# Kernel optimization log

Measured on AMD Instinct MI355X. Metric: run time of the kernel, lower is better.

The kernel has to match this reference:

```python
import jax, jax.numpy as jnp
import numpy as np

GROUPS = 32
EPS = 1e-5


def setup_inputs() -> dict:
    key = jax.random.key(0)
    ks = jax.random.split(key, 8)
    B, C, H, W = 4, 512, 64, 64
    s = 1.0 / np.sqrt(C)  # conv1x1 fan-in init scale
    return {
        "x": jax.random.normal(ks[0], (B, C, H, W), dtype=jnp.float32),
        "gn_gamma": jnp.ones((C,), dtype=jnp.float32),
        "gn_beta": jnp.zeros((C,), dtype=jnp.float32),
        "wq": jax.random.normal(ks[1], (C, C), dtype=jnp.float32) * s,
        "bq": jnp.zeros((C,), dtype=jnp.float32),
        "wk": jax.random.normal(ks[2], (C, C), dtype=jnp.float32) * s,
        "bk": jnp.zeros((C,), dtype=jnp.float32),
        "wv": jax.random.normal(ks[3], (C, C), dtype=jnp.float32) * s,
        "bv": jnp.zeros((C,), dtype=jnp.float32),
    }


def reference(x, gn_gamma, gn_beta, wq, bq, wk, bk, wv, bv):
    B, C, H, W = x.shape
    N = H * W
    # GroupNorm over (channels-within-group, H, W)
    xg = x.reshape(B, GROUPS, C // GROUPS, H, W)
    mean = xg.mean(axis=(2, 3, 4), keepdims=True)
    var = xg.var(axis=(2, 3, 4), keepdims=True)
    xn = ((xg - mean) * jax.lax.rsqrt(var + EPS)).reshape(B, C, H, W)
    xn = xn * gn_gamma[None, :, None, None] + gn_beta[None, :, None, None]
    # 1x1 convs as channel matmuls over flattened spatial tokens: (B, C, N)
    xf = xn.reshape(B, C, N)
    q = jnp.einsum("oc,bcn->bon", wq, xf) + bq[None, :, None]  # (B, Co, N)
    k = jnp.einsum("oc,bcn->bon", wk, xf) + bk[None, :, None]
    v = jnp.einsum("oc,bcn->bon", wv, xf) + bv[None, :, None]
    # scores[b, m, n] = <Q_m, K_n> / sqrt(Co); full N x N matrix as in original
    scale = 1.0 / jnp.sqrt(jnp.asarray(C, dtype=x.dtype))
    scores = jnp.einsum("bcm,bcn->bmn", q, k) * scale  # (B, N, N)
    prob = jax.nn.softmax(scores, axis=-1)
    # out[b, c, m] = sum_n prob[b, m, n] * v[b, c, n]
    attn = jnp.einsum("bmn,bcn->bcm", prob, v).reshape(B, C, H, W)
    return x + attn  # ResLine is Identity since ch_in == ch_out
```

## Files before the change

### kernel.cpp

```cpp
#include <hip/hip_runtime.h>
#include <cstdint>

typedef __attribute__((ext_vector_type(8))) short short8;
typedef __attribute__((ext_vector_type(4))) float floatx4;
typedef __attribute__((ext_vector_type(8))) int intx8;

__device__ __forceinline__ unsigned short f2bf(float f) {
  unsigned int u = __float_as_uint(f);
  u += 0x7fffu + ((u >> 16) & 1u);
  return (unsigned short)(u >> 16);
}

__global__ __launch_bounds__(256) void gn_partial_kernel(
    const float* __restrict__ x, float* __restrict__ gsums) {
  const int b = blockIdx.x >> 8;
  const int g = (blockIdx.x >> 3) & 31;
  const int e = blockIdx.x & 7;
  const long long off = ((long long)(b * 512 + g * 16)) * 4096;
  const float4* xp = (const float4*)(x + off) + e * 2048;
  float s = 0.f, ss = 0.f;
  for (int i = threadIdx.x; i < 2048; i += 256) {
    float4 v = xp[i];
    s  += v.x + v.y + v.z + v.w;
    ss += v.x * v.x + v.y * v.y + v.z * v.z + v.w * v.w;
  }
  for (int off2 = 32; off2; off2 >>= 1) { s += __shfl_down(s, off2); ss += __shfl_down(ss, off2); }
  __shared__ float sb[8];
  const int lane = threadIdx.x & 63, wave = threadIdx.x >> 6;
  if (lane == 0) { sb[wave] = s; sb[4 + wave] = ss; }
  __syncthreads();
  if (threadIdx.x == 0) {
    atomicAdd(gsums + (b * 32 + g) * 2,     sb[0] + sb[1] + sb[2] + sb[3]);
    atomicAdd(gsums + (b * 32 + g) * 2 + 1, sb[4] + sb[5] + sb[6] + sb[7]);
  }
}

__global__ __launch_bounds__(256) void gn_finalize_kernel(
    const float* __restrict__ gsums, const float* __restrict__ gamma,
    const float* __restrict__ beta, float* __restrict__ scale,
    float* __restrict__ shift) {
  const int i = blockIdx.x * 256 + threadIdx.x;
  const int b = i >> 9;
  const int c = i & 511;
  const int g = c >> 4;
  const float S  = gsums[(b * 32 + g) * 2];
  const float SS = gsums[(b * 32 + g) * 2 + 1];
  const float mean = S * (1.f / 65536.f);
  const float var  = SS * (1.f / 65536.f) - mean * mean;
  const float inv  = rsqrtf(var + 1e-5f);
  const float sc = gamma[c] * inv;
  scale[i] = sc;
  shift[i] = beta[c] - mean * sc;
}

__global__ __launch_bounds__(256) void wcvt_zero_kernel(
    const float* __restrict__ wq, const float* __restrict__ wk,
    const float* __restrict__ wv, unsigned short* __restrict__ w16,
    float* __restrict__ zp, int nzero) {
  const int gi = blockIdx.x * 256 + threadIdx.x;
  if (gi < 196608) {
    const int m = gi >> 16;
    const int i = gi & 65535;
    const float* src = (m == 0) ? wq : (m == 1) ? wk : wv;
    float4 v = *((const float4*)src + i);
    ushort4 o;
    o.x = f2bf(v.x); o.y = f2bf(v.y); o.z = f2bf(v.z); o.w = f2bf(v.w);
    *((ushort4*)(w16 + (long long)m * 262144) + i) = o;
  } else {
    const int zi = gi - 196608;
    if (zi < nzero) zp[zi] = 0.f;
  }
}

__global__ __launch_bounds__(256) void norm_transpose_kernel(
    const float* __restrict__ x, const float* __restrict__ scale,
    const float* __restrict__ shift, unsigned short* __restrict__ xnt) {
  const int b = blockIdx.z;
  const int n0 = blockIdx.x * 64;
  const int c0 = blockIdx.y * 64;
  const int t = threadIdx.x;
  __shared__ unsigned short tile[64][65];
  {
    const int cl = t >> 2;
    const int nc = (t & 3) * 16;
    const int c = c0 + cl;
    const float* xp = x + ((long long)b * 512 + c) * 4096 + n0 + nc;
    const float sc = scale[b * 512 + c];
    const float sh = shift[b * 512 + c];
#pragma unroll
    for (int j = 0; j < 16; j += 4) {
      float4 v = *(const float4*)(xp + j);
      tile[cl][nc + j + 0] = f2bf(v.x * sc + sh);
      tile[cl][nc + j + 1] = f2bf(v.y * sc + sh);
      tile[cl][nc + j + 2] = f2bf(v.z * sc + sh);
      tile[cl][nc + j + 3] = f2bf(v.w * sc + sh);
    }
  }
  __syncthreads();
  {
    const int nl = t >> 2;
    const int cc = (t & 3) * 16;
    union { unsigned short u[16]; uint4 q[2]; } o;
#pragma unroll
    for (int j = 0; j < 16; ++j) o.u[j] = tile[cc + j][nl];
    unsigned short* op = xnt + ((long long)b * 4096 + n0 + nl) * 512 + c0 + cc;
    *((uint4*)op) = o.q[0];
    *((uint4*)op + 1) = o.q[1];
  }
}

template <int EPI>
__global__ __launch_bounds__(256) void gemm_tn_kernel(
    const unsigned short* __restrict__ A, const unsigned short* __restrict__ B,
    void* __restrict__ C, const float* __restrict__ bias,
    const float* __restrict__ bias2,
    int lda, int ldb, int ldc, int K,
    long long sA, long long sB, long long sC) {
  const int tid = threadIdx.x;
  const int lane = tid & 63;
  const int wave = tid >> 6;
  const int m0 = blockIdx.x * 128;
  const int n0 = blockIdx.y * 128;
  const int bz = blockIdx.z;
  A += (long long)bz * sA;
  B += (long long)bz * sB;

  __shared__ unsigned short smem[17408];
  unsigned short* As = smem;
  unsigned short* Bs = smem + 8192;

  floatx4 acc[4][4];
#pragma unroll
  for (int i = 0; i < 4; ++i)
#pragma unroll
    for (int j = 0; j < 4; ++j) acc[i][j] = (floatx4){0.f, 0.f, 0.f, 0.f};

  const unsigned short* ag[4];
  const unsigned short* bg[4];
  unsigned ldsoff[4];
#pragma unroll
  for (int i = 0; i < 4; ++i) {
    const int idx = i * 256 + tid;
    const int r = idx >> 3;
    const int g = idx & 7;
    const int gs = g ^ (r & 7);
    ag[i] = A + (long long)(m0 + r) * lda + gs * 8;
    bg[i] = B + (long long)(n0 + r) * ldb + gs * 8;
    ldsoff[i] = (unsigned)(i * 256 + wave * 64) * 8;
  }

  const int l15 = lane & 15;
  const int wm = (wave >> 1) * 64;
  const int wn = (wave & 1) * 64;

  for (int k0 = 0; k0 < K; k0 += 64) {
#pragma unroll
    for (int i = 0; i < 4; ++i) {
      __builtin_amdgcn_global_load_lds(
          (const __attribute__((address_space(1))) void*)(ag[i] + k0),
          (__attribute__((address_space(3))) void*)(As + ldsoff[i]), 16, 0, 0);
      __builtin_amdgcn_global_load_lds(
          (const __attribute__((address_space(1))) void*)(bg[i] + k0),
          (__attribute__((address_space(3))) void*)(Bs + ldsoff[i]), 16, 0, 0);
    }
    __syncthreads();
#pragma unroll
    for (int kk = 0; kk < 64; kk += 32) {
      const int gq = (kk >> 3) + (lane >> 4);
      short8 af[4], bfr[4];
#pragma unroll
      for (int mt = 0; mt < 4; ++mt) {
        const int row = wm + mt * 16 + l15;
        af[mt] = *(const short8*)&As[row * 64 + ((gq ^ (row & 7)) << 3)];
      }
#pragma unroll
      for (int nt = 0; nt < 4; ++nt) {
        const int row = wn + nt * 16 + l15;
        bfr[nt] = *(const short8*)&Bs[row * 64 + ((gq ^ (row & 7)) << 3)];
      }
#pragma unroll
      for (int mt = 0; mt < 4; ++mt)
#pragma unroll
        for (int nt = 0; nt < 4; ++nt)
          acc[mt][nt] = __builtin_amdgcn_mfma_f32_16x16x32_bf16(
              af[mt], bfr[nt], acc[mt][nt], 0, 0, 0);
    }
    __syncthreads();
  }

  const int r0 = (lane >> 4) * 4;

  if (EPI == 6) {
    unsigned char* t8 = (unsigned char*)smem;
    const float* bp = (m0 >= 512) ? bias2 : bias;
    const int mb = m0 & 511;
#pragma unroll
    for (int mt = 0; mt < 4; ++mt) {
      const int ml = wm + mt * 16 + r0;
      const float b0 = bp[mb + ml], b1 = bp[mb + ml + 1];
      const float b2 = bp[mb + ml + 2], b3 = bp[mb + ml + 3];
      const int gw = ml >> 4;
      const int mby = ml & 15;
#pragma unroll
      for (int nt = 0; nt < 4; ++nt) {
        const int nl = wn + nt * 16 + l15;
        int p = __builtin_amdgcn_cvt_pk_fp8_f32(acc[mt][nt][0] + b0,
                                                acc[mt][nt][1] + b1, 0, false);
        p = __builtin_amdgcn_cvt_pk_fp8_f32(acc[mt][nt][2] + b2,
                                            acc[mt][nt][3] + b3, p, true);
        *(int*)&t8[nl * 128 + ((gw ^ (nl & 7)) << 4) + mby] = p;
      }
    }
    __syncthreads();
    unsigned char* o8 = (unsigned char*)C + (long long)bz * sC;
#pragma unroll
    for (int t = 0; t < 4; ++t) {
      const int gid = t * 256 + tid;
      const int row = gid >> 3;
      const int gc = gid & 7;
      uint4 v = *(const uint4*)&t8[row * 128 + ((gc ^ (row & 7)) << 4)];
      *(uint4*)&o8[(long long)(n0 + row) * ldc + m0 + gc * 16] = v;
    }
    return;
  }

  if (EPI == 3) {
    unsigned char* t8 = (unsigned char*)smem;
#pragma unroll
    for (int mt = 0; mt < 4; ++mt) {
      const int ml = wm + mt * 16 + r0;
      const float b0 = bias[m0 + ml],     b1 = bias[m0 + ml + 1];
      const float b2 = bias[m0 + ml + 2], b3 = bias[m0 + ml + 3];
#pragma unroll
      for (int nt = 0; nt < 4; ++nt) {
        const int nl = wn + nt * 16 + l15;
        int p0 = __builtin_amdgcn_cvt_pk_fp8_f32(acc[mt][nt][0] + b0,
                                                 acc[mt][nt][1] + b1, 0, false);
        int p1 = __builtin_amdgcn_cvt_pk_fp8_f32(acc[mt][nt][2] + b2,
                                                 acc[mt][nt][3] + b3, 0, false);
        t8[(ml + 0) * 144 + nl] = (unsigned char)(p0 & 0xff);
        t8[(ml + 1) * 144 + nl] = (unsigned char)((p0 >> 8) & 0xff);
        t8[(ml + 2) * 144 + nl] = (unsigned char)(p1 & 0xff);
        t8[(ml + 3) * 144 + nl] = (unsigned char)((p1 >> 8) & 0xff);
      }
    }
    __syncthreads();
    unsigned char* o8 = (unsigned char*)C + (long long)bz * sC;
#pragma unroll
    for (int t = 0; t < 4; ++t) {
      const int gid = t * 256 + tid;
      const int row = gid >> 3;
      const int gc = gid & 7;
      uint4 v = *(const uint4*)&t8[row * 144 + gc * 16];
      *(uint4*)&o8[(long long)(m0 + row) * ldc + n0 + gc * 16] = v;
    }
    return;
  }
}

__global__ __launch_bounds__(256, 1) void fused_attn_kernel(
    const unsigned char* __restrict__ qk8,
    const unsigned char* __restrict__ vv8,
    float* __restrict__ out, const float* __restrict__ res) {
  const int id = blockIdx.x;
  const int xcd = id & 7;
  const int slot = id >> 3;
  const int bz = xcd & 3;
  const int n0 = ((xcd >> 2) * 32 + slot) * 64;

  const unsigned char* Q = qk8 + (long long)bz * (4096LL * 1024);
  const unsigned char* K = Q + 512;
  const unsigned char* V = vv8 + (long long)bz * (512LL * 4096);

  const int tid = threadIdx.x;
  const int lane = tid & 63;
  const int wave = tid >> 6;
  const int l15 = lane & 15;
  const int quad = lane >> 4;

  __shared__ unsigned char smem[141312];
  unsigned char* Ps = smem + 131072;
  float* red = (float*)(smem + 140288);

  floatx4 acc[8][4];
#pragma unroll
  for (int i = 0; i < 8; ++i)
#pragma unroll
    for (int j = 0; j < 4; ++j) acc[i][j] = (floatx4){0.f, 0.f, 0.f, 0.f};
  float rs[4] = {0.f, 0.f, 0.f, 0.f};

#define FA_GLDS(gp, lp)                                              \
  __builtin_amdgcn_global_load_lds(                                  \
      (const __attribute__((address_space(1))) void*)(gp),           \
      (__attribute__((address_space(3))) void*)(lp), 16, 0, 0)

  const int r8 = tid >> 5;
  const int g5 = tid & 31;
  const int gsw = (g5 & 24) | ((g5 & 7) ^ (r8 & 7));
  const unsigned char* qsrc = Q + (long long)(n0 + r8) * 1024 + gsw * 16;
  const unsigned char* ksrc = K + (long long)r8 * 1024 + gsw * 16;
  const unsigned dstb = (unsigned)wave * 1024;

#pragma unroll
  for (int j = 0; j < 8; ++j)
    FA_GLDS(qsrc + j * 8192, smem + j * 4096 + dstb);
  asm volatile("s_waitcnt vmcnt(0)" ::: "memory");
  __builtin_amdgcn_s_barrier();

  intx8 qf[4][4];
#pragma unroll
  for (int ns = 0; ns < 4; ++ns) {
    const int row = ns * 16 + l15;
    const int r7 = row & 7;
#pragma unroll
    for (int kc = 0; kc < 4; ++kc) {
      const uint4 x0 = *(const uint4*)(smem + row * 512 + kc * 128 +
                                       (((2 * quad) ^ r7) << 4));
      const uint4 x1 = *(const uint4*)(smem + row * 512 + kc * 128 +
                                       (((2 * quad + 1) ^ r7) << 4));
      qf[ns][kc] = (intx8){(int)x0.x, (int)x0.y, (int)x0.z, (int)x0.w,
                           (int)x1.x, (int)x1.y, (int)x1.z, (int)x1.w};
    }
  }
  asm volatile("s_waitcnt lgkmcnt(0)" ::: "memory");
  __builtin_amdgcn_sched_barrier(0);
  __builtin_amdgcn_s_barrier();

#pragma unroll
  for (int j = 0; j < 16; ++j)
    FA_GLDS(ksrc + j * 8192, smem + j * 4096 + dstb);
#pragma unroll
  for (int j = 0; j < 16; ++j)
    FA_GLDS(ksrc + 131072 + j * 8192, smem + 65536 + j * 4096 + dstb);
  asm volatile("s_waitcnt vmcnt(16)" ::: "memory");
  __builtin_amdgcn_s_barrier();

  const unsigned char* vg[8];
#pragma unroll
  for (int cs = 0; cs < 8; ++cs)
    vg[cs] = V + (long long)(wave * 128 + cs * 16 + l15) * 4096 + quad * 32;

  const float SCL = 0.044194173824159216f;

  for (int t = 0; t < 32; ++t) {
    const unsigned char* Kb = smem + (t & 1) * 65536;
    const int jcol = t * 128;

    uint4 vf[8][2];
#pragma unroll
    for (int cs = 0; cs < 8; ++cs) {
      vf[cs][0] = *(const uint4*)(vg[cs] + jcol);
      vf[cs][1] = *(const uint4*)(vg[cs] + jcol + 16);
    }
    __builtin_amdgcn_sched_barrier(0);

    floatx4 sacc[2][4];
#pragma unroll
    for (int mt = 0; mt < 2; ++mt)
#pragma unroll
      for (int ns = 0; ns < 4; ++ns) sacc[mt][ns] = (floatx4){0.f, 0.f, 0.f, 0.f};
#pragma unroll
    for (int kc = 0; kc < 4; ++kc) {
      intx8 kf[2];
#pragma unroll
      for (int mt = 0; mt < 2; ++mt) {
        const int row = wave * 32 + mt * 16 + l15;
        const int r7 = row & 7;
        const uint4 x0 = *(const uint4*)(Kb + row * 512 + kc * 128 +
                                         (((2 * quad) ^ r7) << 4));
        const uint4 x1 = *(const uint4*)(Kb + row * 512 + kc * 128 +
                                         (((2 * quad + 1) ^ r7) << 4));
        kf[mt] = (intx8){(int)x0.x, (int)x0.y, (int)x0.z, (int)x0.w,
                         (int)x1.x, (int)x1.y, (int)x1.z, (int)x1.w};
      }
#pragma unroll
      for (int mt = 0; mt < 2; ++mt)
#pragma unroll
        for (int ns = 0; ns < 4; ++ns)
          sacc[mt][ns] = __builtin_amdgcn_mfma_scale_f32_16x16x128_f8f6f4(
              kf[mt], qf[ns][kc], sacc[mt][ns], 0, 0, 0, 127, 0, 127);
    }

#pragma unroll
    for (int mt = 0; mt < 2; ++mt) {
#pragma unroll
      for (int ns = 0; ns < 4; ++ns) {
        const float e0 = __expf(sacc[mt][ns][0] * SCL);
        const float e1 = __expf(sacc[mt][ns][1] * SCL);
        const float e2 = __expf(sacc[mt][ns][2] * SCL);
        const float e3 = __expf(sacc[mt][ns][3] * SCL);
        rs[ns] += e0 + e1 + e2 + e3;
        int p = __builtin_amdgcn_cvt_pk_fp8_f32(e0, e1, 0, false);
        p = __builtin_amdgcn_cvt_pk_fp8_f32(e2, e3, p, true);
        *(int*)&Ps[(ns * 16 + l15) * 144 + wave * 32 + mt * 16 + quad * 4] = p;
      }
    }
    asm volatile("s_waitcnt lgkmcnt(0)" ::: "memory");
    __builtin_amdgcn_sched_barrier(0);
    __builtin_amdgcn_s_barrier();

    if (t < 30) {
      const unsigned char* ks2 = ksrc + (long long)(t + 2) * 131072;
      unsigned char* db = smem + (t & 1) * 65536;
#pragma unroll
      for (int j = 0; j < 16; ++j)
        FA_GLDS(ks2 + j * 8192, db + j * 4096 + dstb);
    }
    __builtin_amdgcn_sched_barrier(0);

    intx8 pb[4];
#pragma unroll
    for (int ns = 0; ns < 4; ++ns) {
      const int row = ns * 16 + l15;
      const uint4 x0 = *(const uint4*)(Ps + row * 144 + quad * 32);
      const uint4 x1 = *(const uint4*)(Ps + row * 144 + quad * 32 + 16);
      pb[ns] = (intx8){(int)x0.x, (int)x0.y, (int)x0.z, (int)x0.w,
                       (int)x1.x, (int)x1.y, (int)x1.z, (int)x1.w};
    }
    if (t < 30) {
      asm volatile("s_waitcnt vmcnt(16)" ::: "memory");
    } else {
      asm volatile("s_waitcnt vmcnt(0)" ::: "memory");
    }
    __builtin_amdgcn_sched_barrier(0);
    __builtin_amdgcn_s_setprio(1);
#pragma unroll
    for (int cs = 0; cs < 8; ++cs) {
      const intx8 av = (intx8){(int)vf[cs][0].x, (int)vf[cs][0].y,
                               (int)vf[cs][0].z, (int)vf[cs][0].w,
                               (int)vf[cs][1].x, (int)vf[cs][1].y,
                               (int)vf[cs][1].z, (int)vf[cs][1].w};
#pragma unroll
      for (int ns = 0; ns < 4; ++ns)
        acc[cs][ns] = __builtin_amdgcn_mfma_scale_f32_16x16x128_f8f6f4(
            av, pb[ns], acc[cs][ns], 0, 0, 0, 127, 0, 127);
    }
    __builtin_amdgcn_s_setprio(0);
    asm volatile("s_waitcnt lgkmcnt(0)" ::: "memory");
    __builtin_amdgcn_sched_barrier(0);
    __builtin_amdgcn_s_barrier();
  }
#undef FA_GLDS

#pragma unroll
  for (int ns = 0; ns < 4; ++ns) {
    float r = rs[ns];
    r += __shfl_xor(r, 16);
    r += __shfl_xor(r, 32);
    if (quad == 0) red[wave * 64 + ns * 16 + l15] = r;
  }
  __syncthreads();
  float inv[4];
#pragma unroll
  for (int ns = 0; ns < 4; ++ns) {
    float s = 0.f;
#pragma unroll
    for (int w = 0; w < 4; ++w) s += red[w * 64 + ns * 16 + l15];
    inv[ns] = 1.f / s;
  }

  float* o = out + (long long)bz * (4096LL * 512);
  const float* rr = res + (long long)bz * (4096LL * 512);
#pragma unroll
  for (int cs = 0; cs < 8; ++cs) {
#pragma unroll
    for (int ns = 0; ns < 4; ++ns) {
      const int n = n0 + ns * 16 + l15;
#pragma unroll
      for (int r = 0; r < 4; ++r) {
        const int c = wave * 128 + cs * 16 + quad * 4 + r;
        const long long off = (long long)c * 4096 + n;
        o[off] = acc[cs][ns][r] * inv[ns] + rr[off];
      }
    }
  }
}

extern "C" void kernel_launch(void* const* d_in, const int* in_sizes, int n_in,
                              void* d_out, int out_size, void* d_ws, size_t ws_size,
                              hipStream_t stream) {
  const float* x     = (const float*)d_in[0];
  const float* gamma = (const float*)d_in[1];
  const float* beta  = (const float*)d_in[2];
  const float* wq    = (const float*)d_in[3];
  const float* bq    = (const float*)d_in[4];
  const float* wk    = (const float*)d_in[5];
  const float* bk    = (const float*)d_in[6];
  const float* wv    = (const float*)d_in[7];
  const float* bv    = (const float*)d_in[8];
  float* out = (float*)d_out;

  const long long sTok = 4096LL * 512;
  const long long sQK8 = 4096LL * 1024;
  const long long sV8  = 512LL * 4096;

  char* ws = (char*)d_ws;
  float* scale = (float*)ws;
  float* shift = (float*)(ws + 8192);
  unsigned short* w16 = (unsigned short*)(ws + 16384);
  unsigned short* xnt = (unsigned short*)(ws + 1589248);
  unsigned char*  qk8 = (unsigned char*)(ws + 18366464);
  unsigned char*  vv8 = (unsigned char*)(ws + 51920896);
  float* gsums = (float*)(ws + 60317696);

  wcvt_zero_kernel<<<769, 256, 0, stream>>>(wq, wk, wv, w16, gsums, 256);
  gn_partial_kernel<<<1024, 256, 0, stream>>>(x, gsums);
  gn_finalize_kernel<<<8, 256, 0, stream>>>(gsums, gamma, beta, scale, shift);
  norm_transpose_kernel<<<dim3(64, 8, 4), 256, 0, stream>>>(x, scale, shift, xnt);

  gemm_tn_kernel<6><<<dim3(8, 32, 4), 256, 0, stream>>>(
      w16, xnt, qk8, bq, bk, 512, 512, 1024, 512, 0, sTok, sQK8);
  gemm_tn_kernel<3><<<dim3(4, 32, 4), 256, 0, stream>>>(
      w16 + 524288, xnt, vv8, bv, nullptr, 512, 512, 4096, 512, 0, sTok, sV8);

  fused_attn_kernel<<<256, 256, 0, stream>>>(qk8, vv8, out, x);
}
```

Measured before the change: 300.4 us.

## Warp-specialize fused attention into QK/softmax and PV producer-consumer waves

The fused attention kernel is split into two wave groups inside a 512-thread block. Four waves compute QK^T scores and exponentials into a double-buffered P tile, while the other four issue K prefetches and run the PV MFMAs one step behind, forming a software pipeline. The query tile per block drops from 64 to 32 tokens and the grid doubles to 512 blocks. This aims to overlap score computation with the PV matmul, at the cost of K and V being re-read by twice as many blocks. It also adds an extra pipeline step and per-iteration barriers across both groups.

```diff
diff --git a/kernel.cpp b/kernel.cpp
--- a/kernel.cpp
+++ b/kernel.cpp
@@ -258,7 +258,7 @@
   }
 }
 
-__global__ __launch_bounds__(256, 1) void fused_attn_kernel(
+__global__ __launch_bounds__(512, 2) void fused_attn_kernel(
     const unsigned char* __restrict__ qk8,
     const unsigned char* __restrict__ vv8,
     float* __restrict__ out, const float* __restrict__ res) {
@@ -266,7 +266,7 @@
   const int xcd = id & 7;
   const int slot = id >> 3;
   const int bz = xcd & 3;
-  const int n0 = ((xcd >> 2) * 32 + slot) * 64;
+  const int n0 = ((xcd >> 2) * 64 + slot) * 32;
 
   const unsigned char* Q = qk8 + (long long)bz * (4096LL * 1024);
   const unsigned char* K = Q + 512;
@@ -277,200 +277,215 @@
   const int wave = tid >> 6;
   const int l15 = lane & 15;
   const int quad = lane >> 4;
-
-  __shared__ unsigned char smem[141312];
-  unsigned char* Ps = smem + 131072;
+  const bool isQK = wave < 4;
+  const int pw = wave & 3;
+
+  __shared__ unsigned char smem[140800];
   float* red = (float*)(smem + 140288);
 
-  floatx4 acc[8][4];
+  floatx4 acc[8][2];
 #pragma unroll
   for (int i = 0; i < 8; ++i)
 #pragma unroll
-    for (int j = 0; j < 4; ++j) acc[i][j] = (floatx4){0.f, 0.f, 0.f, 0.f};
-  float rs[4] = {0.f, 0.f, 0.f, 0.f};
+    for (int j = 0; j < 2; ++j) acc[i][j] = (floatx4){0.f, 0.f, 0.f, 0.f};
+  float rs[2] = {0.f, 0.f};
 
 #define FA_GLDS(gp, lp)                                              \
   __builtin_amdgcn_global_load_lds(                                  \
       (const __attribute__((address_space(1))) void*)(gp),           \
       (__attribute__((address_space(3))) void*)(lp), 16, 0, 0)
 
-  const int r8 = tid >> 5;
-  const int g5 = tid & 31;
+  const int ltid = tid & 255;
+  const int r8 = ltid >> 5;
+  const int g5 = ltid & 31;
   const int gsw = (g5 & 24) | ((g5 & 7) ^ (r8 & 7));
-  const unsigned char* qsrc = Q + (long long)(n0 + r8) * 1024 + gsw * 16;
-  const unsigned char* ksrc = K + (long long)r8 * 1024 + gsw * 16;
-  const unsigned dstb = (unsigned)wave * 1024;
-
-#pragma unroll
-  for (int j = 0; j < 8; ++j)
-    FA_GLDS(qsrc + j * 8192, smem + j * 4096 + dstb);
+  const unsigned dstb = (unsigned)pw * 1024;
+
+  if (isQK) {
+#pragma unroll
+    for (int j = 0; j < 4; ++j)
+      FA_GLDS(Q + (long long)(n0 + j * 8 + r8) * 1024 + gsw * 16,
+              smem + 65536 + j * 4096 + dstb);
+  } else {
+#pragma unroll
+    for (int j = 0; j < 16; ++j)
+      FA_GLDS(K + (long long)(j * 8 + r8) * 1024 + gsw * 16,
+              smem + j * 4096 + dstb);
+  }
   asm volatile("s_waitcnt vmcnt(0)" ::: "memory");
   __builtin_amdgcn_s_barrier();
 
-  intx8 qf[4][4];
-#pragma unroll
-  for (int ns = 0; ns < 4; ++ns) {
-    const int row = ns * 16 + l15;
-    const int r7 = row & 7;
-#pragma unroll
-    for (int kc = 0; kc < 4; ++kc) {
-      const uint4 x0 = *(const uint4*)(smem + row * 512 + kc * 128 +
-                                       (((2 * quad) ^ r7) << 4));
-      const uint4 x1 = *(const uint4*)(smem + row * 512 + kc * 128 +
-                                       (((2 * quad + 1) ^ r7) << 4));
-      qf[ns][kc] = (intx8){(int)x0.x, (int)x0.y, (int)x0.z, (int)x0.w,
-                           (int)x1.x, (int)x1.y, (int)x1.z, (int)x1.w};
-    }
-  }
-  asm volatile("s_waitcnt lgkmcnt(0)" ::: "memory");
-  __builtin_amdgcn_sched_barrier(0);
-  __builtin_amdgcn_s_barrier();
-
-#pragma unroll
-  for (int j = 0; j < 16; ++j)
-    FA_GLDS(ksrc + j * 8192, smem + j * 4096 + dstb);
-#pragma unroll
-  for (int j = 0; j < 16; ++j)
-    FA_GLDS(ksrc + 131072 + j * 8192, smem + 65536 + j * 4096 + dstb);
-  asm volatile("s_waitcnt vmcnt(16)" ::: "memory");
-  __builtin_amdgcn_s_barrier();
-
-  const unsigned char* vg[8];
-#pragma unroll
-  for (int cs = 0; cs < 8; ++cs)
-    vg[cs] = V + (long long)(wave * 128 + cs * 16 + l15) * 4096 + quad * 32;
-
-  const float SCL = 0.044194173824159216f;
-
-  for (int t = 0; t < 32; ++t) {
-    const unsigned char* Kb = smem + (t & 1) * 65536;
-    const int jcol = t * 128;
-
-    uint4 vf[8][2];
-#pragma unroll
-    for (int cs = 0; cs < 8; ++cs) {
-      vf[cs][0] = *(const uint4*)(vg[cs] + jcol);
-      vf[cs][1] = *(const uint4*)(vg[cs] + jcol + 16);
-    }
-    __builtin_amdgcn_sched_barrier(0);
-
-    floatx4 sacc[2][4];
-#pragma unroll
-    for (int mt = 0; mt < 2; ++mt)
-#pragma unroll
-      for (int ns = 0; ns < 4; ++ns) sacc[mt][ns] = (floatx4){0.f, 0.f, 0.f, 0.f};
-#pragma unroll
-    for (int kc = 0; kc < 4; ++kc) {
-      intx8 kf[2];
-#pragma unroll
-      for (int mt = 0; mt < 2; ++mt) {
-        const int row = wave * 32 + mt * 16 + l15;
-        const int r7 = row & 7;
-        const uint4 x0 = *(const uint4*)(Kb + row * 512 + kc * 128 +
+  intx8 qf[2][4];
+  if (isQK) {
+#pragma unroll
+    for (int ns = 0; ns < 2; ++ns) {
+      const int row = ns * 16 + l15;
+      const int r7 = row & 7;
+#pragma unroll
+      for (int kc = 0; kc < 4; ++kc) {
+        const uint4 x0 = *(const uint4*)(smem + 65536 + row * 512 + kc * 128 +
                                          (((2 * quad) ^ r7) << 4));
-        const uint4 x1 = *(const uint4*)(Kb + row * 512 + kc * 128 +
+        const uint4 x1 = *(const uint4*)(smem + 65536 + row * 512 + kc * 128 +
                                          (((2 * quad + 1) ^ r7) << 4));
-        kf[mt] = (intx8){(int)x0.x, (int)x0.y, (int)x0.z, (int)x0.w,
-                         (int)x1.x, (int)x1.y, (int)x1.z, (int)x1.w};
-      }
-#pragma unroll
-      for (int mt = 0; mt < 2; ++mt)
-#pragma unroll
-        for (int ns = 0; ns < 4; ++ns)
-          sacc[mt][ns] = __builtin_amdgcn_mfma_scale_f32_16x16x128_f8f6f4(
-              kf[mt], qf[ns][kc], sacc[mt][ns], 0, 0, 0, 127, 0, 127);
-    }
-
-#pragma unroll
-    for (int mt = 0; mt < 2; ++mt) {
-#pragma unroll
-      for (int ns = 0; ns < 4; ++ns) {
-        const float e0 = __expf(sacc[mt][ns][0] * SCL);
-        const float e1 = __expf(sacc[mt][ns][1] * SCL);
-        const float e2 = __expf(sacc[mt][ns][2] * SCL);
-        const float e3 = __expf(sacc[mt][ns][3] * SCL);
-        rs[ns] += e0 + e1 + e2 + e3;
-        int p = __builtin_amdgcn_cvt_pk_fp8_f32(e0, e1, 0, false);
-        p = __builtin_amdgcn_cvt_pk_fp8_f32(e2, e3, p, true);
-        *(int*)&Ps[(ns * 16 + l15) * 144 + wave * 32 + mt * 16 + quad * 4] = p;
+        qf[ns][kc] = (intx8){(int)x0.x, (int)x0.y, (int)x0.z, (int)x0.w,
+                             (int)x1.x, (int)x1.y, (int)x1.z, (int)x1.w};
       }
     }
     asm volatile("s_waitcnt lgkmcnt(0)" ::: "memory");
     __builtin_amdgcn_sched_barrier(0);
+  }
+  __builtin_amdgcn_s_barrier();
+
+  const unsigned char* vg[8];
+  if (!isQK) {
+#pragma unroll
+    for (int cs = 0; cs < 8; ++cs)
+      vg[cs] = V + (long long)(pw * 128 + cs * 16 + l15) * 4096 + quad * 32;
+  }
+
+  const float SCL = 0.044194173824159216f;
+
+  for (int t = 0; t <= 32; ++t) {
+    if (isQK) {
+      if (t < 32) {
+        const unsigned char* Kb = smem + (t & 1) * 65536;
+        unsigned char* Pd = smem + 131072 + (t & 1) * 4608;
+        floatx4 sacc[2][2];
+#pragma unroll
+        for (int mt = 0; mt < 2; ++mt)
+#pragma unroll
+          for (int ns = 0; ns < 2; ++ns) sacc[mt][ns] = (floatx4){0.f, 0.f, 0.f, 0.f};
+#pragma unroll
+        for (int kc = 0; kc < 4; ++kc) {
+          intx8 kf[2];
+#pragma unroll
+          for (int mt = 0; mt < 2; ++mt) {
+            const int row = pw * 32 + mt * 16 + l15;
+            const int r7 = row & 7;
+            const uint4 x0 = *(const uint4*)(Kb + row * 512 + kc * 128 +
+                                             (((2 * quad) ^ r7) << 4));
+            const uint4 x1 = *(const uint4*)(Kb + row * 512 + kc * 128 +
+                                             (((2 * quad + 1) ^ r7) << 4));
+            kf[mt] = (intx8){(int)x0.x, (int)x0.y, (int)x0.z, (int)x0.w,
+                             (int)x1.x, (int)x1.y, (int)x1.z, (int)x1.w};
+          }
+#pragma unroll
+          for (int mt = 0; mt < 2; ++mt)
+#pragma unroll
+            for (int ns = 0; ns < 2; ++ns)
+              sacc[mt][ns] = __builtin_amdgcn_mfma_scale_f32_16x16x128_f8f6f4(
+                  kf[mt], qf[ns][kc], sacc[mt][ns], 0, 0, 0, 127, 0, 127);
+        }
+#pragma unroll
+        for (int mt = 0; mt < 2; ++mt) {
+#pragma unroll
+          for (int ns = 0; ns < 2; ++ns) {
+            const float e0 = __expf(sacc[mt][ns][0] * SCL);
+            const float e1 = __expf(sacc[mt][ns][1] * SCL);
+            const float e2 = __expf(sacc[mt][ns][2] * SCL);
+            const float e3 = __expf(sacc[mt][ns][3] * SCL);
+            rs[ns] += e0 + e1 + e2 + e3;
+            int p = __builtin_amdgcn_cvt_pk_fp8_f32(e0, e1, 0, false);
+            p = __builtin_amdgcn_cvt_pk_fp8_f32(e2, e3, p, true);
+            *(int*)&Pd[(ns * 16 + l15) * 144 + pw * 32 + mt * 16 + quad * 4] = p;
+          }
+        }
+        asm volatile("s_waitcnt lgkmcnt(0)" ::: "memory");
+        __builtin_amdgcn_sched_barrier(0);
+      }
+    } else {
+      const bool hasP = (t >= 1);
+      const bool doS = (t <= 30);
+      uint4 vf[8][2];
+      if (hasP) {
+        const int jcol = (t - 1) * 128;
+#pragma unroll
+        for (int cs = 0; cs < 8; ++cs) {
+          vf[cs][0] = *(const uint4*)(vg[cs] + jcol);
+          vf[cs][1] = *(const uint4*)(vg[cs] + jcol + 16);
+        }
+        __builtin_amdgcn_sched_barrier(0);
+      }
+      if (doS) {
+        const unsigned char* ks = K + (long long)(t + 1) * 131072;
+        unsigned char* db = smem + ((t + 1) & 1) * 65536;
+#pragma unroll
+        for (int j = 0; j < 16; ++j)
+          FA_GLDS(ks + (long long)(j * 8 + r8) * 1024 + gsw * 16,
+                  db + j * 4096 + dstb);
+        __builtin_amdgcn_sched_barrier(0);
+      }
+      if (hasP) {
+        if (doS) {
+          asm volatile("s_waitcnt vmcnt(16)" ::: "memory");
+        } else {
+          asm volatile("s_waitcnt vmcnt(0)" ::: "memory");
+        }
+        __builtin_amdgcn_sched_barrier(0);
+        const unsigned char* Pb = smem + 131072 + ((t - 1) & 1) * 4608;
+        intx8 pb[2];
+#pragma unroll
+        for (int ns = 0; ns < 2; ++ns) {
+          const int row = ns * 16 + l15;
+          const uint4 x0 = *(const uint4*)(Pb + row * 144 + quad * 32);
+          const uint4 x1 = *(const uint4*)(Pb + row * 144 + quad * 32 + 16);
+          pb[ns] = (intx8){(int)x0.x, (int)x0.y, (int)x0.z, (int)x0.w,
+                           (int)x1.x, (int)x1.y, (int)x1.z, (int)x1.w};
+        }
+        asm volatile("s_waitcnt lgkmcnt(0)" ::: "memory");
+        __builtin_amdgcn_sched_barrier(0);
+        __builtin_amdgcn_s_setprio(1);
+#pragma unroll
+        for (int cs = 0; cs < 8; ++cs) {
+          const intx8 av = (intx8){(int)vf[cs][0].x, (int)vf[cs][0].y,
+                                   (int)vf[cs][0].z, (int)vf[cs][0].w,
+                                   (int)vf[cs][1].x, (int)vf[cs][1].y,
+                                   (int)vf[cs][1].z, (int)vf[cs][1].w};
+#pragma unroll
+          for (int ns = 0; ns < 2; ++ns)
+            acc[cs][ns] = __builtin_amdgcn_mfma_scale_f32_16x16x128_f8f6f4(
+                av, pb[ns], acc[cs][ns], 0, 0, 0, 127, 0, 127);
+        }
+        __builtin_amdgcn_s_setprio(0);
+      }
+      asm volatile("s_waitcnt vmcnt(0)" ::: "memory");
+    }
     __builtin_amdgcn_s_barrier();
-
-    if (t < 30) {
-      const unsigned char* ks2 = ksrc + (long long)(t + 2) * 131072;
-      unsigned char* db = smem + (t & 1) * 65536;
-#pragma unroll
-      for (int j = 0; j < 16; ++j)
-        FA_GLDS(ks2 + j * 8192, db + j * 4096 + dstb);
-    }
-    __builtin_amdgcn_sched_barrier(0);
-
-    intx8 pb[4];
-#pragma unroll
-    for (int ns = 0; ns < 4; ++ns) {
-      const int row = ns * 16 + l15;
-      const uint4 x0 = *(const uint4*)(Ps + row * 144 + quad * 32);
-      const uint4 x1 = *(const uint4*)(Ps + row * 144 + quad * 32 + 16);
-      pb[ns] = (intx8){(int)x0.x, (int)x0.y, (int)x0.z, (int)x0.w,
-                       (int)x1.x, (int)x1.y, (int)x1.z, (int)x1.w};
-    }
-    if (t < 30) {
-      asm volatile("s_waitcnt vmcnt(16)" ::: "memory");
-    } else {
-      asm volatile("s_waitcnt vmcnt(0)" ::: "memory");
-    }
-    __builtin_amdgcn_sched_barrier(0);
-    __builtin_amdgcn_s_setprio(1);
+  }
+#undef FA_GLDS
+
+  if (isQK) {
+#pragma unroll
+    for (int ns = 0; ns < 2; ++ns) {
+      float r = rs[ns];
+      r += __shfl_xor(r, 16);
+      r += __shfl_xor(r, 32);
+      if (quad == 0) red[pw * 32 + ns * 16 + l15] = r;
+    }
+  }
+  __syncthreads();
+  if (!isQK) {
+    float inv[2];
+#pragma unroll
+    for (int ns = 0; ns < 2; ++ns) {
+      float s = 0.f;
+#pragma unroll
+      for (int w = 0; w < 4; ++w) s += red[w * 32 + ns * 16 + l15];
+      inv[ns] = 1.f / s;
+    }
+    float* o = out + (long long)bz * (4096LL * 512);
+    const float* rr = res + (long long)bz * (4096LL * 512);
 #pragma unroll
     for (int cs = 0; cs < 8; ++cs) {
-      const intx8 av = (intx8){(int)vf[cs][0].x, (int)vf[cs][0].y,
-                               (int)vf[cs][0].z, (int)vf[cs][0].w,
-                               (int)vf[cs][1].x, (int)vf[cs][1].y,
-                               (int)vf[cs][1].z, (int)vf[cs][1].w};
-#pragma unroll
-      for (int ns = 0; ns < 4; ++ns)
-        acc[cs][ns] = __builtin_amdgcn_mfma_scale_f32_16x16x128_f8f6f4(
-            av, pb[ns], acc[cs][ns], 0, 0, 0, 127, 0, 127);
-    }
-    __builtin_amdgcn_s_setprio(0);
-    asm volatile("s_waitcnt lgkmcnt(0)" ::: "memory");
-    __builtin_amdgcn_sched_barrier(0);
-    __builtin_amdgcn_s_barrier();
-  }
-#undef FA_GLDS
-
-#pragma unroll
-  for (int ns = 0; ns < 4; ++ns) {
-    float r = rs[ns];
-    r += __shfl_xor(r, 16);
-    r += __shfl_xor(r, 32);
-    if (quad == 0) red[wave * 64 + ns * 16 + l15] = r;
-  }
-  __syncthreads();
-  float inv[4];
-#pragma unroll
-  for (int ns = 0; ns < 4; ++ns) {
-    float s = 0.f;
-#pragma unroll
-    for (int w = 0; w < 4; ++w) s += red[w * 64 + ns * 16 + l15];
-    inv[ns] = 1.f / s;
-  }
-
-  float* o = out + (long long)bz * (4096LL * 512);
-  const float* rr = res + (long long)bz * (4096LL * 512);
-#pragma unroll
-  for (int cs = 0; cs < 8; ++cs) {
-#pragma unroll
-    for (int ns = 0; ns < 4; ++ns) {
-      const int n = n0 + ns * 16 + l15;
-#pragma unroll
-      for (int r = 0; r < 4; ++r) {
-        const int c = wave * 128 + cs * 16 + quad * 4 + r;
-        const long long off = (long long)c * 4096 + n;
-        o[off] = acc[cs][ns][r] * inv[ns] + rr[off];
+#pragma unroll
+      for (int ns = 0; ns < 2; ++ns) {
+        const int n = n0 + ns * 16 + l15;
+#pragma unroll
+        for (int r = 0; r < 4; ++r) {
+          const int c = pw * 128 + cs * 16 + quad * 4 + r;
+          const long long off = (long long)c * 4096 + n;
+          o[off] = acc[cs][ns][r] * inv[ns] + rr[off];
+        }
       }
     }
   }
@@ -513,5 +528,5 @@
   gemm_tn_kernel<3><<<dim3(4, 32, 4), 256, 0, stream>>>(
       w16 + 524288, xnt, vv8, bv, nullptr, 512, 512, 4096, 512, 0, sTok, sV8);
 
-  fused_attn_kernel<<<256, 256, 0, stream>>>(qk8, vv8, out, x);
-}
+  fused_attn_kernel<<<512, 512, 0, stream>>>(qk8, vv8, out, x);
+}
```

New measurement: 338.3 us. 1.13x slower.
